# Optimization experiments

Measured on AMD Instinct MI355X. Metric: run time of the kernel, lower is better.

## Reference

```python
import jax, jax.numpy as jnp
import numpy as np

C_Z = 128
C_H = 128
EPS = 1e-5


def _layer_norm(x, gamma, beta):
    mu = jnp.mean(x, axis=-1, keepdims=True)
    var = jnp.mean(jnp.square(x - mu), axis=-1, keepdims=True)
    return (x - mu) * jax.lax.rsqrt(var + EPS) * gamma + beta


def setup_inputs() -> dict:
    key = jax.random.key(0)
    ks = jax.random.split(key, 8)
    B, N = 1, 512
    s_z = 1.0 / np.sqrt(C_Z)
    s_h = 1.0 / np.sqrt(C_H)
    return {
        "z": jax.random.normal(ks[0], (B, N, N, C_Z), dtype=jnp.float32),
        "mask": jnp.ones((B, N, N), dtype=jnp.float32),
        # linear_ab_p: c_z -> 2*c_hidden
        "w_ab_p": jax.random.normal(ks[1], (2 * C_H, C_Z), dtype=jnp.float32) * s_z,
        "b_ab_p": jnp.zeros((2 * C_H,), dtype=jnp.float32),
        # linear_ab_g: c_z -> 2*c_hidden (gating init)
        "w_ab_g": jax.random.normal(ks[2], (2 * C_H, C_Z), dtype=jnp.float32) * s_z,
        "b_ab_g": jnp.ones((2 * C_H,), dtype=jnp.float32),
        # linear_g: c_z -> c_z (gating init)
        "w_g": jax.random.normal(ks[3], (C_Z, C_Z), dtype=jnp.float32) * s_z,
        "b_g": jnp.ones((C_Z,), dtype=jnp.float32),
        # linear_z: c_hidden -> c_z (final init)
        "w_z": jax.random.normal(ks[4], (C_Z, C_H), dtype=jnp.float32) * s_h,
        "b_z": jnp.zeros((C_Z,), dtype=jnp.float32),
        # layer norms
        "ln_in_g": jnp.ones((C_Z,), dtype=jnp.float32),
        "ln_in_b": jnp.zeros((C_Z,), dtype=jnp.float32),
        "ln_out_g": jnp.ones((C_H,), dtype=jnp.float32),
        "ln_out_b": jnp.zeros((C_H,), dtype=jnp.float32),
    }


def reference(z, mask, w_ab_p, b_ab_p, w_ab_g, b_ab_g, w_g, b_g, w_z, b_z,
              ln_in_g, ln_in_b, ln_out_g, ln_out_b):
    # [B, N, N, C] pair representation; outgoing triangle update
    zn = _layer_norm(z, ln_in_g, ln_in_b)
    m = mask[..., None]  # [B, N, N, 1]
    # gated dual projections: sigmoid(W_g z) * mask * (W_p z)  -> [B, N, N, 2H]
    gate = jax.nn.sigmoid(jnp.einsum("bijc,hc->bijh", zn, w_ab_g) + b_ab_g) * m
    ab = gate * (jnp.einsum("bijc,hc->bijh", zn, w_ab_p) + b_ab_p)
    a, b = jnp.split(ab, 2, axis=-1)  # each [B, N, N, H]
    # outgoing: x[b,i,j,h] = sum_k a[b,i,k,h] * b[b,j,k,h]
    x = jnp.einsum("bikh,bjkh->bijh", a, b)
    x = _layer_norm(x, ln_out_g, ln_out_b)
    out = (jnp.einsum("bijh,ch->bijc", x, w_z) + b_z)
    g = jax.nn.sigmoid(jnp.einsum("bijc,dc->bijd", zn, w_g) + b_g)
    return out * g
```

## Files before the change

kernel.cpp:

```cpp
#include <hip/hip_runtime.h>
#include <math.h>

#define NN 512
#define RR 262144
#define EPS_F 1e-5f

typedef unsigned short u16;
typedef unsigned int u32;
typedef __bf16 bf16x8 __attribute__((ext_vector_type(8)));
typedef float f32x4 __attribute__((ext_vector_type(4)));

__device__ __forceinline__ u16 f2bs(float f) {
  __bf16 h = (__bf16)f;
  return __builtin_bit_cast(u16, h);
}
__device__ __forceinline__ float bs2f(u16 u) {
  return (float)__builtin_bit_cast(__bf16, u);
}
__device__ __forceinline__ float sigmoidf_(float x) {
  return 1.f / (1.f + __expf(-x));
}

__global__ __launch_bounds__(256) void k_ln_in(const float* __restrict__ z,
                                               const float* __restrict__ g,
                                               const float* __restrict__ b,
                                               u16* __restrict__ zn) {
  const int w = threadIdx.x >> 6, l = threadIdx.x & 63;
  const long r = (long)blockIdx.x * 4 + w;
  const float2 v = *(const float2*)(z + r * 128 + l * 2);
  float s = v.x + v.y, sq = v.x * v.x + v.y * v.y;
#pragma unroll
  for (int m = 1; m < 64; m <<= 1) {
    s += __shfl_xor(s, m);
    sq += __shfl_xor(sq, m);
  }
  const float mu = s * 0.0078125f;
  const float var = sq * 0.0078125f - mu * mu;
  const float rs = rsqrtf(var + EPS_F);
  const float2 gg = *(const float2*)(g + l * 2);
  const float2 bb = *(const float2*)(b + l * 2);
  const u32 o = (u32)f2bs((v.x - mu) * rs * gg.x + bb.x) |
                ((u32)f2bs((v.y - mu) * rs * gg.y + bb.y) << 16);
  *(u32*)(zn + r * 128 + l * 2) = o;
}

__global__ __launch_bounds__(256) void k_proj(
    const u16* __restrict__ zn, const float* __restrict__ mask,
    const float* __restrict__ w_ab_p, const float* __restrict__ b_ab_p,
    const float* __restrict__ w_ab_g, const float* __restrict__ b_ab_g,
    const float* __restrict__ w_g, const float* __restrict__ b_g,
    u16* __restrict__ a_t, u16* __restrict__ b_t, u16* __restrict__ g_out) {
  __shared__ __align__(16) u16 As[128 * 136];
  __shared__ __align__(16) u16 Bs[128 * 136];
  __shared__ float maskS[128];
  const int t = threadIdx.x;
  const int tt = blockIdx.y;
  const long row0 = (long)blockIdx.x * 128;

  {
    const int row = t >> 1, half = t & 1;
    const uint4* src = (const uint4*)(zn + (row0 + row) * 128 + half * 64);
    uint4* dst = (uint4*)(As + row * 136 + half * 64);
#pragma unroll
    for (int i = 0; i < 8; ++i) dst[i] = src[i];
  }
  {
    const int n = t >> 1, half = t & 1;
    const float* src;
    if (tt < 4) {
      const int srow = tt * 64 + ((n >> 5) << 4) + (n & 15);
      src = (((n >> 4) & 1) ? w_ab_g : w_ab_p) + srow * 128 + half * 64;
    } else {
      src = w_g + n * 128 + half * 64;
    }
    u16* dst = Bs + n * 136 + half * 64;
#pragma unroll
    for (int i = 0; i < 16; ++i) {
      const float4 v = *(const float4*)(src + i * 4);
      dst[i * 4 + 0] = f2bs(v.x);
      dst[i * 4 + 1] = f2bs(v.y);
      dst[i * 4 + 2] = f2bs(v.z);
      dst[i * 4 + 3] = f2bs(v.w);
    }
  }
  if (t < 128) maskS[t] = mask[row0 + t];
  __syncthreads();

  const int lane = t & 63, wv = t >> 6;
  const int quad = lane >> 4, tl = lane & 15;
  const int wm = wv >> 1, wn = wv & 1;
  f32x4 acc[4][4];
#pragma unroll
  for (int mt = 0; mt < 4; ++mt)
#pragma unroll
    for (int nt = 0; nt < 4; ++nt) acc[mt][nt] = (f32x4){0.f, 0.f, 0.f, 0.f};

#pragma unroll
  for (int ks = 0; ks < 4; ++ks) {
    bf16x8 af[4], bfr[4];
#pragma unroll
    for (int mt = 0; mt < 4; ++mt)
      af[mt] = *(const bf16x8*)(As + (wm * 64 + mt * 16 + tl) * 136 + ks * 32 + quad * 8);
#pragma unroll
    for (int nt = 0; nt < 4; ++nt)
      bfr[nt] = *(const bf16x8*)(Bs + (wn * 64 + nt * 16 + tl) * 136 + ks * 32 + quad * 8);
#pragma unroll
    for (int mt = 0; mt < 4; ++mt)
#pragma unroll
      for (int nt = 0; nt < 4; ++nt)
        acc[mt][nt] = __builtin_amdgcn_mfma_f32_16x16x32_bf16(af[mt], bfr[nt], acc[mt][nt], 0, 0, 0);
  }

  if (tt < 4) {
    __syncthreads();
    u16* trans = As;
#pragma unroll
    for (int b2 = 0; b2 < 2; ++b2) {
      const int hl = wn * 32 + b2 * 16 + tl;
      const int hg = tt * 64 + hl;
      const float bp = b_ab_p[hg], bg = b_ab_g[hg];
#pragma unroll
      for (int mt = 0; mt < 4; ++mt) {
#pragma unroll
        for (int rg = 0; rg < 4; ++rg) {
          const int r = wm * 64 + mt * 16 + quad * 4 + rg;
          const float p = acc[mt][2 * b2][rg] + bp;
          const float gt = acc[mt][2 * b2 + 1][rg] + bg;
          trans[hl * 136 + r] = f2bs(sigmoidf_(gt) * maskS[r] * p);
        }
      }
    }
    __syncthreads();
    const int hl = t >> 2, qq = t & 3;
    const int hg = tt * 64 + hl;
    u16* dbuf = (tt < 2) ? a_t : b_t;
    const int hb = (tt < 2) ? hg : hg - 128;
    const uint4* src = (const uint4*)(trans + hl * 136 + qq * 32);
    uint4* dst = (uint4*)(dbuf + (long)hb * RR + row0 + qq * 32);
#pragma unroll
    for (int i = 0; i < 4; ++i) dst[i] = src[i];
  } else {
#pragma unroll
    for (int nt = 0; nt < 4; ++nt) {
      const int c = wn * 64 + nt * 16 + tl;
      const float bgc = b_g[c];
#pragma unroll
      for (int mt = 0; mt < 4; ++mt)
#pragma unroll
        for (int rg = 0; rg < 4; ++rg) {
          const int r = wm * 64 + mt * 16 + quad * 4 + rg;
          g_out[(row0 + r) * (long)128 + c] = f2bs(sigmoidf_(acc[mt][nt][rg] + bgc));
        }
    }
  }
}

__global__ __launch_bounds__(256) void k_tri(const u16* __restrict__ a_t,
                                             const u16* __restrict__ b_t,
                                             u16* __restrict__ x_t) {
  __shared__ __align__(16) u16 As[128 * 72];
  __shared__ __align__(16) u16 Bs[128 * 72];
  const int t = threadIdx.x;
  const int h = blockIdx.y;
  const int i0 = (blockIdx.x >> 2) * 128, j0 = (blockIdx.x & 3) * 128;
  const u16* Ag = a_t + (long)h * RR;
  const u16* Bg = b_t + (long)h * RR;
  const int lane = t & 63, wv = t >> 6;
  const int quad = lane >> 4, tl = lane & 15;
  const int wm = wv >> 1, wn = wv & 1;
  const int chunk = t & 7, rb = t >> 3;

  f32x4 acc[4][4];
#pragma unroll
  for (int mt = 0; mt < 4; ++mt)
#pragma unroll
    for (int nt = 0; nt < 4; ++nt) acc[mt][nt] = (f32x4){0.f, 0.f, 0.f, 0.f};

  for (int kt = 0; kt < 8; ++kt) {
    __syncthreads();
#pragma unroll
    for (int p = 0; p < 4; ++p) {
      const int row = rb + p * 32;
      *(uint4*)(As + row * 72 + chunk * 8) =
          *(const uint4*)(Ag + (long)(i0 + row) * 512 + kt * 64 + chunk * 8);
      *(uint4*)(Bs + row * 72 + chunk * 8) =
          *(const uint4*)(Bg + (long)(j0 + row) * 512 + kt * 64 + chunk * 8);
    }
    __syncthreads();
#pragma unroll
    for (int ks = 0; ks < 2; ++ks) {
      bf16x8 af[4], bfr[4];
#pragma unroll
      for (int mt = 0; mt < 4; ++mt)
        af[mt] = *(const bf16x8*)(As + (wm * 64 + mt * 16 + tl) * 72 + ks * 32 + quad * 8);
#pragma unroll
      for (int nt = 0; nt < 4; ++nt)
        bfr[nt] = *(const bf16x8*)(Bs + (wn * 64 + nt * 16 + tl) * 72 + ks * 32 + quad * 8);
#pragma unroll
      for (int mt = 0; mt < 4; ++mt)
#pragma unroll
        for (int nt = 0; nt < 4; ++nt)
          acc[mt][nt] = __builtin_amdgcn_mfma_f32_16x16x32_bf16(af[mt], bfr[nt], acc[mt][nt], 0, 0, 0);
    }
  }
#pragma unroll
  for (int mt = 0; mt < 4; ++mt)
#pragma unroll
    for (int nt = 0; nt < 4; ++nt)
#pragma unroll
      for (int rg = 0; rg < 4; ++rg) {
        const int i = i0 + wm * 64 + mt * 16 + quad * 4 + rg;
        const int j = j0 + wn * 64 + nt * 16 + tl;
        x_t[(long)h * RR + (long)i * 512 + j] = f2bs(acc[mt][nt][rg]);
      }
}

__global__ __launch_bounds__(256) void k_out(const u16* __restrict__ x_t,
                                             const float* __restrict__ w_z,
                                             const float* __restrict__ b_z,
                                             const float* __restrict__ ln_g,
                                             const float* __restrict__ ln_b,
                                             const u16* __restrict__ g_in,
                                             float* __restrict__ out) {
  __shared__ __align__(16) u16 Xs[128 * 136];
  __shared__ __align__(16) u16 Ws[128 * 136];
  __shared__ float lnGs[128], lnBs[128];
  const int t = threadIdx.x;
  const long row0 = (long)blockIdx.x * 128;

  if (t < 128) {
    lnGs[t] = ln_g[t];
    lnBs[t] = ln_b[t];
  }
  {
    const int hb = t >> 3, rq = t & 7;
    u32 xv[4][8];
#pragma unroll
    for (int hh = 0; hh < 4; ++hh) {
      const uint4* src = (const uint4*)(x_t + (long)(hb * 4 + hh) * RR + row0 + rq * 16);
      const uint4 a = src[0], b = src[1];
      xv[hh][0] = a.x; xv[hh][1] = a.y; xv[hh][2] = a.z; xv[hh][3] = a.w;
      xv[hh][4] = b.x; xv[hh][5] = b.y; xv[hh][6] = b.z; xv[hh][7] = b.w;
    }
#pragma unroll
    for (int rr = 0; rr < 16; ++rr) {
      const int wi = rr >> 1, sh = (rr & 1) * 16;
      const u32 e0 = (xv[0][wi] >> sh) & 0xffffu;
      const u32 e1 = (xv[1][wi] >> sh) & 0xffffu;
      const u32 e2 = (xv[2][wi] >> sh) & 0xffffu;
      const u32 e3 = (xv[3][wi] >> sh) & 0xffffu;
      *(uint2*)(Xs + (rq * 16 + rr) * 136 + hb * 4) = make_uint2(e0 | (e1 << 16), e2 | (e3 << 16));
    }
  }
  {
    const int n = t >> 1, half = t & 1;
    const float* src = w_z + n * 128 + half * 64;
    u16* dst = Ws + n * 136 + half * 64;
#pragma unroll
    for (int i = 0; i < 16; ++i) {
      const float4 v = *(const float4*)(src + i * 4);
      dst[i * 4 + 0] = f2bs(v.x);
      dst[i * 4 + 1] = f2bs(v.y);
      dst[i * 4 + 2] = f2bs(v.z);
      dst[i * 4 + 3] = f2bs(v.w);
    }
  }
  __syncthreads();
  {
    const int r = t >> 1, half = t & 1;
    u16* xr = Xs + r * 136 + half * 64;
    float vals[64];
    float s = 0.f, sq = 0.f;
#pragma unroll
    for (int i = 0; i < 64; ++i) {
      const float v = bs2f(xr[i]);
      vals[i] = v;
      s += v;
      sq += v * v;
    }
    s += __shfl_xor(s, 1);
    sq += __shfl_xor(sq, 1);
    const float mu = s * 0.0078125f;
    const float var = sq * 0.0078125f - mu * mu;
    const float rs = rsqrtf(var + EPS_F);
#pragma unroll
    for (int i = 0; i < 64; ++i) {
      const int hh = half * 64 + i;
      xr[i] = f2bs((vals[i] - mu) * rs * lnGs[hh] + lnBs[hh]);
    }
  }
  __syncthreads();

  const int lane = t & 63, wv = t >> 6;
  const int quad = lane >> 4, tl = lane & 15;
  const int wm = wv >> 1, wn = wv & 1;
  f32x4 acc[4][4];
#pragma unroll
  for (int mt = 0; mt < 4; ++mt)
#pragma unroll
    for (int nt = 0; nt < 4; ++nt) acc[mt][nt] = (f32x4){0.f, 0.f, 0.f, 0.f};

#pragma unroll
  for (int ks = 0; ks < 4; ++ks) {
    bf16x8 af[4], bfr[4];
#pragma unroll
    for (int mt = 0; mt < 4; ++mt)
      af[mt] = *(const bf16x8*)(Xs + (wm * 64 + mt * 16 + tl) * 136 + ks * 32 + quad * 8);
#pragma unroll
    for (int nt = 0; nt < 4; ++nt)
      bfr[nt] = *(const bf16x8*)(Ws + (wn * 64 + nt * 16 + tl) * 136 + ks * 32 + quad * 8);
#pragma unroll
    for (int mt = 0; mt < 4; ++mt)
#pragma unroll
      for (int nt = 0; nt < 4; ++nt)
        acc[mt][nt] = __builtin_amdgcn_mfma_f32_16x16x32_bf16(af[mt], bfr[nt], acc[mt][nt], 0, 0, 0);
  }
#pragma unroll
  for (int nt = 0; nt < 4; ++nt) {
    const int c = wn * 64 + nt * 16 + tl;
    const float bz = b_z[c];
#pragma unroll
    for (int mt = 0; mt < 4; ++mt)
#pragma unroll
      for (int rg = 0; rg < 4; ++rg) {
        const int r = wm * 64 + mt * 16 + quad * 4 + rg;
        const long idx = (row0 + r) * 128 + c;
        out[idx] = (acc[mt][nt][rg] + bz) * bs2f(g_in[idx]);
      }
  }
}

extern "C" void kernel_launch(void* const* d_in, const int* in_sizes, int n_in,
                              void* d_out, int out_size, void* d_ws, size_t ws_size,
                              hipStream_t stream) {
  const float* z = (const float*)d_in[0];
  const float* mask = (const float*)d_in[1];
  const float* w_ab_p = (const float*)d_in[2];
  const float* b_ab_p = (const float*)d_in[3];
  const float* w_ab_g = (const float*)d_in[4];
  const float* b_ab_g = (const float*)d_in[5];
  const float* w_g = (const float*)d_in[6];
  const float* b_g = (const float*)d_in[7];
  const float* w_z = (const float*)d_in[8];
  const float* b_z = (const float*)d_in[9];
  const float* ln_in_g = (const float*)d_in[10];
  const float* ln_in_b = (const float*)d_in[11];
  const float* ln_out_g = (const float*)d_in[12];
  const float* ln_out_b = (const float*)d_in[13];
  float* out = (float*)d_out;

  u16* zn = (u16*)d_ws;
  u16* a_t = zn + (size_t)RR * 128;
  u16* b_t = a_t + (size_t)RR * 128;
  u16* x_t = b_t + (size_t)RR * 128;
  u16* g_b = x_t + (size_t)RR * 128;

  k_ln_in<<<RR / 4, 256, 0, stream>>>(z, ln_in_g, ln_in_b, zn);
  k_proj<<<dim3(RR / 128, 5), 256, 0, stream>>>(zn, mask, w_ab_p, b_ab_p, w_ab_g,
                                                b_ab_g, w_g, b_g, a_t, b_t, g_b);
  k_tri<<<dim3(16, 128), 256, 0, stream>>>(a_t, b_t, x_t);
  k_out<<<RR / 128, 256, 0, stream>>>(x_t, w_z, b_z, ln_out_g, ln_out_b, g_b, out);
}
```

Baseline: 580.4 us.

## Pre-convert weights once, use async global-to-LDS copies with XOR-swizzled layouts

Adds a small kernel that converts all projection weights to bf16 once, folding the output LayerNorm gamma into w_z and precomputing the correction vectors. The projection and output GEMMs now read B fragments straight from global memory instead of re-converting weights into LDS in every block. The output LayerNorm is applied algebraically in the epilogue using per-row mean and rstd. The activation tiles in k_proj and k_tri are loaded with global_load_lds async copies into unpadded XOR-swizzled LDS, which means zn and a_t/b_t are written pre-swizzled; launch bounds are raised for occupancy. The risks are uncached global B-fragment reads and correctness of the swizzle indexing.

After: 616.9 us. 1.06x slower.

```diff
diff --git a/kernel.cpp b/kernel.cpp
--- a/kernel.cpp
+++ b/kernel.cpp
@@ -19,6 +19,51 @@
 }
 __device__ __forceinline__ float sigmoidf_(float x) {
   return 1.f / (1.f + __expf(-x));
+}
+__device__ __forceinline__ void async_copy16(const u16* g, u16* l) {
+  __builtin_amdgcn_global_load_lds(
+      (const __attribute__((address_space(1))) u32*)g,
+      (__attribute__((address_space(3))) u32*)l, 16, 0, 0);
+}
+
+__global__ __launch_bounds__(256) void k_wconv(
+    const float* __restrict__ w_ab_p, const float* __restrict__ w_ab_g,
+    const float* __restrict__ w_g, const float* __restrict__ w_z,
+    const float* __restrict__ b_z, const float* __restrict__ ln_out_g,
+    const float* __restrict__ ln_out_b, u16* __restrict__ wb,
+    float* __restrict__ uv) {
+  if (blockIdx.x < 96) {
+    const int u = blockIdx.x * 256 + threadIdx.x;
+    const int row = u >> 5;
+    const int c4 = (u & 31) * 4;
+    float4 v;
+    if (row < 512) {
+      const int tt = row >> 7, n = row & 127;
+      const int srow = tt * 64 + ((n >> 5) << 4) + (n & 15);
+      v = *(const float4*)((((n >> 4) & 1) ? w_ab_g : w_ab_p) + srow * 128 + c4);
+    } else if (row < 640) {
+      v = *(const float4*)(w_g + (row - 512) * 128 + c4);
+    } else {
+      const int c = row - 640;
+      v = *(const float4*)(w_z + c * 128 + c4);
+      const float4 gv = *(const float4*)(ln_out_g + c4);
+      v.x *= gv.x; v.y *= gv.y; v.z *= gv.z; v.w *= gv.w;
+    }
+    u16 o[4] = {f2bs(v.x), f2bs(v.y), f2bs(v.z), f2bs(v.w)};
+    *(uint2*)(wb + row * 128 + c4) = *(uint2*)o;
+  } else {
+    const int t = threadIdx.x;
+    const int c = t & 127;
+    const float* wr = w_z + c * 128;
+    float s = 0.f;
+    if (t < 128) {
+      for (int h = 0; h < 128; ++h) s += ln_out_g[h] * wr[h];
+      uv[c] = s;
+    } else {
+      for (int h = 0; h < 128; ++h) s += ln_out_b[h] * wr[h];
+      uv[128 + c] = s + b_z[c];
+    }
+  }
 }
 
 __global__ __launch_bounds__(256) void k_ln_in(const float* __restrict__ z,
@@ -41,52 +86,34 @@
   const float2 bb = *(const float2*)(b + l * 2);
   const u32 o = (u32)f2bs((v.x - mu) * rs * gg.x + bb.x) |
                 ((u32)f2bs((v.y - mu) * rs * gg.y + bb.y) << 16);
-  *(u32*)(zn + r * 128 + l * 2) = o;
-}
-
-__global__ __launch_bounds__(256) void k_proj(
+  const int c = l >> 2;
+  const int slot = (c & 8) | ((c & 7) ^ ((int)r & 7));
+  *(u32*)(zn + r * 128 + slot * 8 + 2 * (l & 3)) = o;
+}
+
+__global__ __launch_bounds__(256, 4) void k_proj(
     const u16* __restrict__ zn, const float* __restrict__ mask,
-    const float* __restrict__ w_ab_p, const float* __restrict__ b_ab_p,
-    const float* __restrict__ w_ab_g, const float* __restrict__ b_ab_g,
-    const float* __restrict__ w_g, const float* __restrict__ b_g,
+    const u16* __restrict__ wb, const float* __restrict__ b_ab_p,
+    const float* __restrict__ b_ab_g, const float* __restrict__ b_g,
     u16* __restrict__ a_t, u16* __restrict__ b_t, u16* __restrict__ g_out) {
-  __shared__ __align__(16) u16 As[128 * 136];
-  __shared__ __align__(16) u16 Bs[128 * 136];
+  __shared__ __align__(16) u16 As[128 * 128];
   __shared__ float maskS[128];
   const int t = threadIdx.x;
   const int tt = blockIdx.y;
   const long row0 = (long)blockIdx.x * 128;
+  const int lane = t & 63, wv = t >> 6;
 
   {
-    const int row = t >> 1, half = t & 1;
-    const uint4* src = (const uint4*)(zn + (row0 + row) * 128 + half * 64);
-    uint4* dst = (uint4*)(As + row * 136 + half * 64);
-#pragma unroll
-    for (int i = 0; i < 8; ++i) dst[i] = src[i];
-  }
-  {
-    const int n = t >> 1, half = t & 1;
-    const float* src;
-    if (tt < 4) {
-      const int srow = tt * 64 + ((n >> 5) << 4) + (n & 15);
-      src = (((n >> 4) & 1) ? w_ab_g : w_ab_p) + srow * 128 + half * 64;
-    } else {
-      src = w_g + n * 128 + half * 64;
-    }
-    u16* dst = Bs + n * 136 + half * 64;
-#pragma unroll
-    for (int i = 0; i < 16; ++i) {
-      const float4 v = *(const float4*)(src + i * 4);
-      dst[i * 4 + 0] = f2bs(v.x);
-      dst[i * 4 + 1] = f2bs(v.y);
-      dst[i * 4 + 2] = f2bs(v.z);
-      dst[i * 4 + 3] = f2bs(v.w);
+#pragma unroll
+    for (int q = 0; q < 8; ++q) {
+      const int chunk = wv * 8 + q;
+      const int row = chunk * 4 + (lane >> 4);
+      async_copy16(zn + (row0 + row) * 128 + (lane & 15) * 8, As + chunk * 512);
     }
   }
   if (t < 128) maskS[t] = mask[row0 + t];
   __syncthreads();
 
-  const int lane = t & 63, wv = t >> 6;
   const int quad = lane >> 4, tl = lane & 15;
   const int wm = wv >> 1, wn = wv & 1;
   f32x4 acc[4][4];
@@ -95,15 +122,18 @@
 #pragma unroll
     for (int nt = 0; nt < 4; ++nt) acc[mt][nt] = (f32x4){0.f, 0.f, 0.f, 0.f};
 
+  const u16* wrow = wb + (long)tt * 128 * 128;
 #pragma unroll
   for (int ks = 0; ks < 4; ++ks) {
     bf16x8 af[4], bfr[4];
+    const int cA = ks * 4 + quad;
+    const int slotA = (cA & 8) | ((cA & 7) ^ (tl & 7));
 #pragma unroll
     for (int mt = 0; mt < 4; ++mt)
-      af[mt] = *(const bf16x8*)(As + (wm * 64 + mt * 16 + tl) * 136 + ks * 32 + quad * 8);
+      af[mt] = *(const bf16x8*)(As + (wm * 64 + mt * 16 + tl) * 128 + slotA * 8);
 #pragma unroll
     for (int nt = 0; nt < 4; ++nt)
-      bfr[nt] = *(const bf16x8*)(Bs + (wn * 64 + nt * 16 + tl) * 136 + ks * 32 + quad * 8);
+      bfr[nt] = *(const bf16x8*)(wrow + (wn * 64 + nt * 16 + tl) * 128 + ks * 32 + quad * 8);
 #pragma unroll
     for (int mt = 0; mt < 4; ++mt)
 #pragma unroll
@@ -113,7 +143,7 @@
 
   if (tt < 4) {
     __syncthreads();
-    u16* trans = As;
+    u16* Ts = As;
 #pragma unroll
     for (int b2 = 0; b2 < 2; ++b2) {
       const int hl = wn * 32 + b2 * 16 + tl;
@@ -121,24 +151,33 @@
       const float bp = b_ab_p[hg], bg = b_ab_g[hg];
 #pragma unroll
       for (int mt = 0; mt < 4; ++mt) {
+        u16 pk[4];
 #pragma unroll
         for (int rg = 0; rg < 4; ++rg) {
           const int r = wm * 64 + mt * 16 + quad * 4 + rg;
           const float p = acc[mt][2 * b2][rg] + bp;
           const float gt = acc[mt][2 * b2 + 1][rg] + bg;
-          trans[hl * 136 + r] = f2bs(sigmoidf_(gt) * maskS[r] * p);
+          pk[rg] = f2bs(sigmoidf_(gt) * maskS[r] * p);
         }
+        *(uint2*)(Ts + hl * 136 + wm * 64 + mt * 16 + quad * 4) = *(uint2*)pk;
       }
     }
     __syncthreads();
-    const int hl = t >> 2, qq = t & 3;
-    const int hg = tt * 64 + hl;
-    u16* dbuf = (tt < 2) ? a_t : b_t;
-    const int hb = (tt < 2) ? hg : hg - 128;
-    const uint4* src = (const uint4*)(trans + hl * 136 + qq * 32);
-    uint4* dst = (uint4*)(dbuf + (long)hb * RR + row0 + qq * 32);
-#pragma unroll
-    for (int i = 0; i < 4; ++i) dst[i] = src[i];
+    {
+      const int hl = t >> 2, qq = t & 3;
+      const int hg = tt * 64 + hl;
+      u16* dbuf = (tt < 2) ? a_t : b_t;
+      const int hb = (tt < 2) ? hg : hg - 128;
+      const int i7 = (blockIdx.x >> 2) & 7;
+      const int k0c = ((int)row0 & 511) >> 3;
+      const long base = (long)hb * RR + (row0 & ~(long)511);
+#pragma unroll
+      for (int ii = 0; ii < 4; ++ii) {
+        const int lc = qq * 4 + ii;
+        const int slot = k0c + (lc & 8) + ((lc & 7) ^ i7);
+        *(uint4*)(dbuf + base + slot * 8) = *(const uint4*)(Ts + hl * 136 + lc * 8);
+      }
+    }
   } else {
 #pragma unroll
     for (int nt = 0; nt < 4; ++nt) {
@@ -155,11 +194,11 @@
   }
 }
 
-__global__ __launch_bounds__(256) void k_tri(const u16* __restrict__ a_t,
-                                             const u16* __restrict__ b_t,
-                                             u16* __restrict__ x_t) {
-  __shared__ __align__(16) u16 As[128 * 72];
-  __shared__ __align__(16) u16 Bs[128 * 72];
+__global__ __launch_bounds__(256, 4) void k_tri(const u16* __restrict__ a_t,
+                                                const u16* __restrict__ b_t,
+                                                u16* __restrict__ x_t) {
+  __shared__ __align__(16) u16 As[128 * 64];
+  __shared__ __align__(16) u16 Bs[128 * 64];
   const int t = threadIdx.x;
   const int h = blockIdx.y;
   const int i0 = (blockIdx.x >> 2) * 128, j0 = (blockIdx.x & 3) * 128;
@@ -168,7 +207,6 @@
   const int lane = t & 63, wv = t >> 6;
   const int quad = lane >> 4, tl = lane & 15;
   const int wm = wv >> 1, wn = wv & 1;
-  const int chunk = t & 7, rb = t >> 3;
 
   f32x4 acc[4][4];
 #pragma unroll
@@ -179,23 +217,24 @@
   for (int kt = 0; kt < 8; ++kt) {
     __syncthreads();
 #pragma unroll
-    for (int p = 0; p < 4; ++p) {
-      const int row = rb + p * 32;
-      *(uint4*)(As + row * 72 + chunk * 8) =
-          *(const uint4*)(Ag + (long)(i0 + row) * 512 + kt * 64 + chunk * 8);
-      *(uint4*)(Bs + row * 72 + chunk * 8) =
-          *(const uint4*)(Bg + (long)(j0 + row) * 512 + kt * 64 + chunk * 8);
+    for (int q = 0; q < 4; ++q) {
+      const int chunk = wv * 4 + q;
+      const int row = chunk * 8 + (lane >> 3);
+      const int kof = kt * 64 + (lane & 7) * 8;
+      async_copy16(Ag + (long)(i0 + row) * 512 + kof, As + chunk * 512);
+      async_copy16(Bg + (long)(j0 + row) * 512 + kof, Bs + chunk * 512);
     }
     __syncthreads();
 #pragma unroll
     for (int ks = 0; ks < 2; ++ks) {
       bf16x8 af[4], bfr[4];
+      const int slot = (ks * 4 + quad) ^ (tl & 7);
 #pragma unroll
       for (int mt = 0; mt < 4; ++mt)
-        af[mt] = *(const bf16x8*)(As + (wm * 64 + mt * 16 + tl) * 72 + ks * 32 + quad * 8);
+        af[mt] = *(const bf16x8*)(As + (wm * 64 + mt * 16 + tl) * 64 + slot * 8);
 #pragma unroll
       for (int nt = 0; nt < 4; ++nt)
-        bfr[nt] = *(const bf16x8*)(Bs + (wn * 64 + nt * 16 + tl) * 72 + ks * 32 + quad * 8);
+        bfr[nt] = *(const bf16x8*)(Bs + (wn * 64 + nt * 16 + tl) * 64 + slot * 8);
 #pragma unroll
       for (int mt = 0; mt < 4; ++mt)
 #pragma unroll
@@ -215,23 +254,16 @@
       }
 }
 
-__global__ __launch_bounds__(256) void k_out(const u16* __restrict__ x_t,
-                                             const float* __restrict__ w_z,
-                                             const float* __restrict__ b_z,
-                                             const float* __restrict__ ln_g,
-                                             const float* __restrict__ ln_b,
-                                             const u16* __restrict__ g_in,
-                                             float* __restrict__ out) {
+__global__ __launch_bounds__(256, 4) void k_out(const u16* __restrict__ x_t,
+                                                const u16* __restrict__ w2,
+                                                const float* __restrict__ uv,
+                                                const u16* __restrict__ g_in,
+                                                float* __restrict__ out) {
   __shared__ __align__(16) u16 Xs[128 * 136];
-  __shared__ __align__(16) u16 Ws[128 * 136];
-  __shared__ float lnGs[128], lnBs[128];
+  __shared__ float muS[128], rsS[128];
   const int t = threadIdx.x;
   const long row0 = (long)blockIdx.x * 128;
 
-  if (t < 128) {
-    lnGs[t] = ln_g[t];
-    lnBs[t] = ln_b[t];
-  }
   {
     const int hb = t >> 3, rq = t & 7;
     u32 xv[4][8];
@@ -242,51 +274,43 @@
       xv[hh][0] = a.x; xv[hh][1] = a.y; xv[hh][2] = a.z; xv[hh][3] = a.w;
       xv[hh][4] = b.x; xv[hh][5] = b.y; xv[hh][6] = b.z; xv[hh][7] = b.w;
     }
+    const int cslot0 = (hb >> 1) + rq * 2;
+    const int hoff = (hb & 1) * 4;
 #pragma unroll
     for (int rr = 0; rr < 16; ++rr) {
+      const int row = rq * 16 + rr;
       const int wi = rr >> 1, sh = (rr & 1) * 16;
       const u32 e0 = (xv[0][wi] >> sh) & 0xffffu;
       const u32 e1 = (xv[1][wi] >> sh) & 0xffffu;
       const u32 e2 = (xv[2][wi] >> sh) & 0xffffu;
       const u32 e3 = (xv[3][wi] >> sh) & 0xffffu;
-      *(uint2*)(Xs + (rq * 16 + rr) * 136 + hb * 4) = make_uint2(e0 | (e1 << 16), e2 | (e3 << 16));
-    }
-  }
-  {
-    const int n = t >> 1, half = t & 1;
-    const float* src = w_z + n * 128 + half * 64;
-    u16* dst = Ws + n * 136 + half * 64;
-#pragma unroll
-    for (int i = 0; i < 16; ++i) {
-      const float4 v = *(const float4*)(src + i * 4);
-      dst[i * 4 + 0] = f2bs(v.x);
-      dst[i * 4 + 1] = f2bs(v.y);
-      dst[i * 4 + 2] = f2bs(v.z);
-      dst[i * 4 + 3] = f2bs(v.w);
+      *(uint2*)(Xs + row * 136 + (cslot0 & 15) * 8 + hoff) =
+          make_uint2(e0 | (e1 << 16), e2 | (e3 << 16));
     }
   }
   __syncthreads();
   {
     const int r = t >> 1, half = t & 1;
-    u16* xr = Xs + r * 136 + half * 64;
-    float vals[64];
+    const int rot = (r >> 4) * 2;
     float s = 0.f, sq = 0.f;
 #pragma unroll
-    for (int i = 0; i < 64; ++i) {
-      const float v = bs2f(xr[i]);
-      vals[i] = v;
-      s += v;
-      sq += v * v;
+    for (int j = 0; j < 8; ++j) {
+      const int c = half * 8 + j;
+      const bf16x8 v8 = *(const bf16x8*)(Xs + r * 136 + ((c + rot) & 15) * 8);
+#pragma unroll
+      for (int e = 0; e < 8; ++e) {
+        const float v = (float)v8[e];
+        s += v;
+        sq += v * v;
+      }
     }
     s += __shfl_xor(s, 1);
     sq += __shfl_xor(sq, 1);
-    const float mu = s * 0.0078125f;
-    const float var = sq * 0.0078125f - mu * mu;
-    const float rs = rsqrtf(var + EPS_F);
-#pragma unroll
-    for (int i = 0; i < 64; ++i) {
-      const int hh = half * 64 + i;
-      xr[i] = f2bs((vals[i] - mu) * rs * lnGs[hh] + lnBs[hh]);
+    if (half == 0) {
+      const float mu = s * 0.0078125f;
+      const float var = sq * 0.0078125f - mu * mu;
+      muS[r] = mu;
+      rsS[r] = rsqrtf(var + EPS_F);
     }
   }
   __syncthreads();
@@ -303,12 +327,15 @@
 #pragma unroll
   for (int ks = 0; ks < 4; ++ks) {
     bf16x8 af[4], bfr[4];
-#pragma unroll
-    for (int mt = 0; mt < 4; ++mt)
-      af[mt] = *(const bf16x8*)(Xs + (wm * 64 + mt * 16 + tl) * 136 + ks * 32 + quad * 8);
+    const int c = ks * 4 + quad;
+#pragma unroll
+    for (int mt = 0; mt < 4; ++mt) {
+      const int rot = (wm * 4 + mt) * 2;
+      af[mt] = *(const bf16x8*)(Xs + (wm * 64 + mt * 16 + tl) * 136 + ((c + rot) & 15) * 8);
+    }
 #pragma unroll
     for (int nt = 0; nt < 4; ++nt)
-      bfr[nt] = *(const bf16x8*)(Ws + (wn * 64 + nt * 16 + tl) * 136 + ks * 32 + quad * 8);
+      bfr[nt] = *(const bf16x8*)(w2 + (wn * 64 + nt * 16 + tl) * 128 + ks * 32 + quad * 8);
 #pragma unroll
     for (int mt = 0; mt < 4; ++mt)
 #pragma unroll
@@ -318,14 +345,14 @@
 #pragma unroll
   for (int nt = 0; nt < 4; ++nt) {
     const int c = wn * 64 + nt * 16 + tl;
-    const float bz = b_z[c];
+    const float uc = uv[c], vc = uv[128 + c];
 #pragma unroll
     for (int mt = 0; mt < 4; ++mt)
 #pragma unroll
       for (int rg = 0; rg < 4; ++rg) {
         const int r = wm * 64 + mt * 16 + quad * 4 + rg;
         const long idx = (row0 + r) * 128 + c;
-        out[idx] = (acc[mt][nt][rg] + bz) * bs2f(g_in[idx]);
+        out[idx] = (rsS[r] * (acc[mt][nt][rg] - muS[r] * uc) + vc) * bs2f(g_in[idx]);
       }
   }
 }
@@ -354,10 +381,14 @@
   u16* b_t = a_t + (size_t)RR * 128;
   u16* x_t = b_t + (size_t)RR * 128;
   u16* g_b = x_t + (size_t)RR * 128;
-
+  u16* wb = g_b + (size_t)RR * 128;
+  float* uv = (float*)(wb + 768 * 128);
+
+  k_wconv<<<97, 256, 0, stream>>>(w_ab_p, w_ab_g, w_g, w_z, b_z, ln_out_g,
+                                  ln_out_b, wb, uv);
   k_ln_in<<<RR / 4, 256, 0, stream>>>(z, ln_in_g, ln_in_b, zn);
-  k_proj<<<dim3(RR / 128, 5), 256, 0, stream>>>(zn, mask, w_ab_p, b_ab_p, w_ab_g,
-                                                b_ab_g, w_g, b_g, a_t, b_t, g_b);
+  k_proj<<<dim3(RR / 128, 5), 256, 0, stream>>>(zn, mask, wb, b_ab_p, b_ab_g,
+                                                b_g, a_t, b_t, g_b);
   k_tri<<<dim3(16, 128), 256, 0, stream>>>(a_t, b_t, x_t);
-  k_out<<<RR / 128, 256, 0, stream>>>(x_t, w_z, b_z, ln_out_g, ln_out_b, g_b, out);
-}
+  k_out<<<RR / 128, 256, 0, stream>>>(x_t, wb + 640 * 128, uv, g_b, out);
+}
```
